# Optimization experiments

Measured on AMD Instinct MI355X. Metric: run time of the kernel, lower is better.

Reference implementation:

```python
import jax, jax.numpy as jnp
import numpy as np

B, C, NH = 2, 128, 4
H = W = D = 28
WS = 7
SHIFT = 3
N = WS * WS * WS            # 343 tokens per window
HD = C // NH                # 32
SCALE = HD ** -0.5
HIDDEN = int(C * 4.0)
EPS = 1e-5


def _rel_pos_index():
    coords = np.stack(np.meshgrid(np.arange(WS), np.arange(WS), np.arange(WS), indexing='ij'))
    cf = coords.reshape(3, -1)                      # (3, N)
    rel = cf[:, :, None] - cf[:, None, :]           # (3, N, N)
    rel = rel.transpose(1, 2, 0) + (WS - 1)         # (N, N, 3), shifted to >=0
    idx = rel[..., 0] * (2 * WS - 1) ** 2 + rel[..., 1] * (2 * WS - 1) + rel[..., 2]
    return jnp.asarray(idx, dtype=jnp.int32)        # (N, N)


def setup_inputs() -> dict:
    key = jax.random.key(0)
    ks = jax.random.split(key, 16)
    s = 0.02
    return {
        'x': jax.random.normal(ks[0], (B, H * W * D, C), jnp.float32),
        'norm1_w': jnp.ones((C,), jnp.float32),
        'norm1_b': jnp.zeros((C,), jnp.float32),
        'qkv_w': jax.random.normal(ks[1], (3 * C, C), jnp.float32) * s,
        'qkv_b': jnp.zeros((3 * C,), jnp.float32),
        'rpb_table': jax.random.normal(ks[2], ((2 * WS - 1) ** 3, NH), jnp.float32) * s,
        'proj_w': jax.random.normal(ks[3], (C, C), jnp.float32) * s,
        'proj_b': jnp.zeros((C,), jnp.float32),
        'norm2_w': jnp.ones((C,), jnp.float32),
        'norm2_b': jnp.zeros((C,), jnp.float32),
        'mlp_w1': jax.random.normal(ks[4], (HIDDEN, C), jnp.float32) * s,
        'mlp_b1': jnp.zeros((HIDDEN,), jnp.float32),
        'mlp_w2': jax.random.normal(ks[5], (C, HIDDEN), jnp.float32) * s,
        'mlp_b2': jnp.zeros((C,), jnp.float32),
        'rel_idx': _rel_pos_index(),
    }


def _layernorm(x, w, b):
    mu = jnp.mean(x, axis=-1, keepdims=True)
    var = jnp.mean(jnp.square(x - mu), axis=-1, keepdims=True)
    return (x - mu) * jax.lax.rsqrt(var + EPS) * w + b


def _window_partition(x):
    # (B,H,W,D,C) -> (B*nW, N, C)
    x = x.reshape(B, H // WS, WS, W // WS, WS, D // WS, WS, C)
    x = x.transpose(0, 1, 3, 5, 2, 4, 6, 7)
    return x.reshape(-1, N, C)


def _window_reverse(wins):
    # (B*nW, N, C) -> (B,H,W,D,C)
    x = wins.reshape(B, H // WS, W // WS, D // WS, WS, WS, WS, C)
    x = x.transpose(0, 1, 4, 2, 5, 3, 6, 7)
    return x.reshape(B, H, W, D, C)


def _window_attention(xw, qkv_w, qkv_b, rpb_table, rel_idx, proj_w, proj_b):
    Bw = xw.shape[0]
    qkv = xw @ qkv_w.T + qkv_b                       # (Bw, N, 3C)
    qkv = qkv.reshape(Bw, N, 3, NH, HD).transpose(2, 0, 3, 1, 4)
    q, k, v = qkv[0], qkv[1], qkv[2]                 # each (Bw, NH, N, HD)
    attn = jnp.einsum('bhnd,bhmd->bhnm', q * SCALE, k)
    bias = rpb_table[rel_idx.reshape(-1)].reshape(N, N, NH).transpose(2, 0, 1)
    attn = jax.nn.softmax(attn + bias[None], axis=-1)
    out = jnp.einsum('bhnm,bhmd->bhnd', attn, v)     # (Bw, NH, N, HD)
    out = out.transpose(0, 2, 1, 3).reshape(Bw, N, C)
    return out @ proj_w.T + proj_b


def reference(x, norm1_w, norm1_b, qkv_w, qkv_b, rpb_table, proj_w, proj_b,
              norm2_w, norm2_b, mlp_w1, mlp_b1, mlp_w2, mlp_b2, rel_idx):
    shortcut = x
    h = _layernorm(x, norm1_w, norm1_b).reshape(B, H, W, D, C)
    if SHIFT > 0:
        h = jnp.roll(h, shift=(-SHIFT, -SHIFT, -SHIFT), axis=(1, 2, 3))
    wins = _window_partition(h)
    wins = _window_attention(wins, qkv_w, qkv_b, rpb_table, rel_idx, proj_w, proj_b)
    h = _window_reverse(wins)
    if SHIFT > 0:
        h = jnp.roll(h, shift=(SHIFT, SHIFT, SHIFT), axis=(1, 2, 3))
    x = shortcut + h.reshape(B, H * W * D, C)
    m = _layernorm(x, norm2_w, norm2_b)
    m = jax.nn.gelu(m @ mlp_w1.T + mlp_b1, approximate=False) @ mlp_w2.T + mlp_b2
    return x + m
```

## Files before the change

kernel.cpp:

```cpp
#include <hip/hip_runtime.h>

typedef __bf16 bfv8 __attribute__((ext_vector_type(8)));
typedef float f32x4 __attribute__((ext_vector_type(4)));
#define MFMA16(a,b,c) __builtin_amdgcn_mfma_f32_16x16x32_bf16(a,b,c,0,0,0)

constexpr int C      = 128;
constexpr int HD     = 32;
constexpr int NTOK   = 343;
constexpr int ROWS   = 43904;
constexpr int HIDDEN = 512;
constexpr float SCALE = 0.17677669529663687f;
constexpr float EPS   = 1e-5f;
constexpr int NT = 22;

static __device__ __forceinline__ float b2f(ushort u) {
  union { unsigned int i; float f; } x; x.i = ((unsigned int)u) << 16; return x.f;
}
static __device__ __forceinline__ ushort f2b(float f) {
  union { float f; unsigned int i; } x; x.f = f;
  unsigned int r = x.i + 0x7fffu + ((x.i >> 16) & 1u);
  return (ushort)(r >> 16);
}

static __device__ __forceinline__ int perm_row(int row) {
  int win = row / NTOK, tok = row - win * NTOK;
  int bb = win >> 6, wi = win & 63;
  int a  = wi >> 4, w2 = (wi >> 2) & 3, c2 = wi & 3;
  int t1 = tok / 49, rem = tok - t1 * 49;
  int t2 = rem / 7,  t3 = rem - t2 * 7;
  int gh = a * 7 + t1 + 3;  if (gh >= 28) gh -= 28;
  int gw = w2 * 7 + t2 + 3; if (gw >= 28) gw -= 28;
  int gd = c2 * 7 + t3 + 3; if (gd >= 28) gd -= 28;
  return bb * 21952 + gh * 784 + gw * 28 + gd;
}

__global__ __launch_bounds__(256) void cvt_kernel(const float* __restrict__ s0,
                                                  const float* __restrict__ s1,
                                                  const float* __restrict__ s2,
                                                  const float* __restrict__ s3,
                                                  ushort* __restrict__ d0,
                                                  ushort* __restrict__ d1,
                                                  ushort* __restrict__ d2,
                                                  ushort* __restrict__ d3) {
  int t = blockIdx.x * 256 + threadIdx.x;
  if (t < 49152)       d0[t]          = f2b(s0[t]);
  else if (t < 65536)  d1[t - 49152]  = f2b(s1[t - 49152]);
  else if (t < 131072) d2[t - 65536]  = f2b(s2[t - 65536]);
  else                 d3[t - 131072] = f2b(s3[t - 131072]);
}

__global__ __launch_bounds__(256) void bias_kernel(const int* __restrict__ rel,
                                                   const float* __restrict__ tab,
                                                   float4* __restrict__ biasr) {
  int t = blockIdx.x * 256 + threadIdx.x;
  if (t >= 4 * NT * NT * 64) return;
  int lane = t & 63;
  int nt   = (t >> 6) % NT;
  int mt   = ((t >> 6) / NT) % NT;
  int head = t / (64 * NT * NT);
  int k  = nt * 16 + (lane & 15);
  int qb = mt * 16 + (lane >> 4) * 4;
  float vv[4];
  #pragma unroll
  for (int r = 0; r < 4; ++r) {
    int q = qb + r;
    if (q < NTOK && k < NTOK) {
      int idx = rel[q * NTOK + k];
      vv[r] = tab[idx * 4 + head];
    } else {
      vv[r] = -3e38f;
    }
  }
  biasr[t] = make_float4(vv[0], vv[1], vv[2], vv[3]);
}

template<bool PERM>
__global__ __launch_bounds__(256) void ln_kernel(const float* __restrict__ in,
                                                 const float* __restrict__ w,
                                                 const float* __restrict__ b,
                                                 ushort* __restrict__ out) {
  int wid = threadIdx.x >> 6, lane = threadIdx.x & 63;
  int row = blockIdx.x * 4 + wid;
  int src = PERM ? perm_row(row) : row;
  float2 v = *reinterpret_cast<const float2*>(in + (size_t)src * C + lane * 2);
  float s = v.x + v.y, q = v.x * v.x + v.y * v.y;
  #pragma unroll
  for (int off = 32; off; off >>= 1) { s += __shfl_xor(s, off); q += __shfl_xor(q, off); }
  float mu = s * (1.0f / 128.0f);
  float var = q * (1.0f / 128.0f) - mu * mu;
  float rs = rsqrtf(var + EPS);
  int c = lane * 2;
  ushort2 ov;
  ov.x = f2b((v.x - mu) * rs * w[c]     + b[c]);
  ov.y = f2b((v.y - mu) * rs * w[c + 1] + b[c + 1]);
  *reinterpret_cast<ushort2*>(out + (size_t)row * C + c) = ov;
}

template<int KTOT, int EPI>
__global__ __launch_bounds__(256) void gemm_kernel(const ushort* __restrict__ A,
                                                   const ushort* __restrict__ W,
                                                   const float* __restrict__ bias,
                                                   const float* __restrict__ X,
                                                   ushort* __restrict__ O0,
                                                   ushort* __restrict__ O1,
                                                   ushort* __restrict__ O2,
                                                   float* __restrict__ OF) {
  __shared__ ushort Al[128][136];
  __shared__ ushort Bl[128][136];
  const int m0 = blockIdx.x * 128, n0 = blockIdx.y * 128;
  const int tid = threadIdx.x, lane = tid & 63, wid = tid >> 6;
  const int wr = wid >> 1, wc = wid & 1;
  const int lr = lane & 15, kb0 = (lane >> 4) * 8;
  const int sr = tid >> 4, sc = (tid & 15) * 8;
  f32x4 acc[4][4] = {};
  for (int kc = 0; kc < KTOT; kc += 128) {
    #pragma unroll
    for (int p = 0; p < 8; ++p) {
      int row = p * 16 + sr;
      *reinterpret_cast<int4*>(&Al[row][sc]) =
          *reinterpret_cast<const int4*>(&A[(size_t)(m0 + row) * KTOT + kc + sc]);
      *reinterpret_cast<int4*>(&Bl[row][sc]) =
          *reinterpret_cast<const int4*>(&W[(size_t)(n0 + row) * KTOT + kc + sc]);
    }
    __syncthreads();
    #pragma unroll
    for (int kk = 0; kk < 4; ++kk) {
      int kb = kk * 32 + kb0;
      bfv8 a[4], b[4];
      #pragma unroll
      for (int m = 0; m < 4; ++m) a[m] = *reinterpret_cast<const bfv8*>(&Al[wr * 64 + m * 16 + lr][kb]);
      #pragma unroll
      for (int n = 0; n < 4; ++n) b[n] = *reinterpret_cast<const bfv8*>(&Bl[wc * 64 + n * 16 + lr][kb]);
      #pragma unroll
      for (int m = 0; m < 4; ++m)
        #pragma unroll
        for (int n = 0; n < 4; ++n)
          acc[m][n] = MFMA16(a[m], b[n], acc[m][n]);
    }
    __syncthreads();
  }
  #pragma unroll
  for (int m = 0; m < 4; ++m)
    #pragma unroll
    for (int n = 0; n < 4; ++n)
      #pragma unroll
      for (int r = 0; r < 4; ++r) {
        int gm = m0 + wr * 64 + m * 16 + (lane >> 4) * 4 + r;
        int gn = n0 + wc * 64 + n * 16 + (lane & 15);
        float v = acc[m][n][r] + bias[gn];
        if (EPI == 0) {
          int which = gn >> 7, head = (gn >> 5) & 3, d = gn & 31;
          if (which == 0) v *= SCALE;
          int win = gm / NTOK, tok = gm - win * NTOK;
          ushort* dst = (which == 0) ? O0 : (which == 1) ? O1 : O2;
          dst[((win * 4 + head) * NTOK + tok) * HD + d] = f2b(v);
        } else if (EPI == 1) {
          int orig = perm_row(gm);
          OF[(size_t)orig * C + gn] = v + X[(size_t)orig * C + gn];
        } else if (EPI == 2) {
          float g = 0.5f * v * (1.0f + erff(v * 0.70710678118654752f));
          O0[(size_t)gm * HIDDEN + gn] = f2b(g);
        } else {
          OF[(size_t)gm * C + gn] = v + X[(size_t)gm * C + gn];
        }
      }
}

__global__ __launch_bounds__(512) void attn_kernel(const ushort* __restrict__ Q,
                                                   const ushort* __restrict__ K,
                                                   const ushort* __restrict__ V,
                                                   const f32x4* __restrict__ biasr,
                                                   ushort* __restrict__ out) {
  __shared__ ushort vt[32][360];
  __shared__ ushort pl[8][16][204];
  const int wh = blockIdx.x;
  const int win = wh >> 2, head = wh & 3;
  const int tid = threadIdx.x, lane = tid & 63, wave = tid >> 6;
  if (tid < 352) {
    int t = tid;
    if (t < NTOK) {
      ushort tmp[32];
      const ushort* vr = V + ((size_t)wh * NTOK + t) * HD;
      *reinterpret_cast<int4*>(&tmp[0])  = *reinterpret_cast<const int4*>(vr);
      *reinterpret_cast<int4*>(&tmp[8])  = *reinterpret_cast<const int4*>(vr + 8);
      *reinterpret_cast<int4*>(&tmp[16]) = *reinterpret_cast<const int4*>(vr + 16);
      *reinterpret_cast<int4*>(&tmp[24]) = *reinterpret_cast<const int4*>(vr + 24);
      #pragma unroll
      for (int d = 0; d < 32; ++d) vt[d][t] = tmp[d];
    } else {
      #pragma unroll
      for (int d = 0; d < 32; ++d) vt[d][t] = 0;
    }
  }
  __syncthreads();
  const int lr = lane & 15, kb0 = (lane >> 4) * 8;
  const int key = lane & 15, qr4 = (lane >> 4) * 4;
  for (int mt = wave; mt < NT; mt += 8) {
    int qrow = mt * 16 + lr; if (qrow > 342) qrow = 342;
    bfv8 aq = *reinterpret_cast<const bfv8*>(Q + ((size_t)wh * NTOK + qrow) * HD + kb0);
    const f32x4* bR = biasr + ((size_t)(head * NT + mt) * NT) * 64 + lane;
    float sm[4] = {0.f, 0.f, 0.f, 0.f};
    f32x4 o0 = {}, o1 = {};
    #pragma unroll
    for (int nt = 0; nt < 12; ++nt) {
      int krow = nt * 16 + lr;
      bfv8 bk = *reinterpret_cast<const bfv8*>(K + ((size_t)wh * NTOK + krow) * HD + kb0);
      f32x4 s = MFMA16(aq, bk, bR[nt * 64]);
      int kcol = nt * 16 + key;
      #pragma unroll
      for (int r = 0; r < 4; ++r) {
        float p = __expf(s[r]);
        sm[r] += p;
        pl[wave][qr4 + r][kcol] = f2b(p);
      }
    }
    #pragma unroll
    for (int kt = 0; kt < 6; ++kt) {
      bfv8 bp  = *reinterpret_cast<const bfv8*>(&pl[wave][lr][kt * 32 + kb0]);
      bfv8 av0 = *reinterpret_cast<const bfv8*>(&vt[lr][kt * 32 + kb0]);
      bfv8 av1 = *reinterpret_cast<const bfv8*>(&vt[16 + lr][kt * 32 + kb0]);
      o0 = MFMA16(av0, bp, o0);
      o1 = MFMA16(av1, bp, o1);
    }
    #pragma unroll
    for (int nt = 12; nt < NT; ++nt) {
      int krow = nt * 16 + lr; if (krow > 342) krow = 342;
      bfv8 bk = *reinterpret_cast<const bfv8*>(K + ((size_t)wh * NTOK + krow) * HD + kb0);
      f32x4 s = MFMA16(aq, bk, bR[nt * 64]);
      int kcol = (nt - 12) * 16 + key;
      #pragma unroll
      for (int r = 0; r < 4; ++r) {
        float p = __expf(s[r]);
        sm[r] += p;
        pl[wave][qr4 + r][kcol] = f2b(p);
      }
    }
    #pragma unroll
    for (int kt = 0; kt < 5; ++kt) {
      bfv8 bp  = *reinterpret_cast<const bfv8*>(&pl[wave][lr][kt * 32 + kb0]);
      bfv8 av0 = *reinterpret_cast<const bfv8*>(&vt[lr][192 + kt * 32 + kb0]);
      bfv8 av1 = *reinterpret_cast<const bfv8*>(&vt[16 + lr][192 + kt * 32 + kb0]);
      o0 = MFMA16(av0, bp, o0);
      o1 = MFMA16(av1, bp, o1);
    }
    #pragma unroll
    for (int r = 0; r < 4; ++r) {
      #pragma unroll
      for (int off = 1; off < 16; off <<= 1) sm[r] += __shfl_xor(sm[r], off);
    }
    float inv[4];
    #pragma unroll
    for (int r = 0; r < 4; ++r) inv[r] = 1.0f / sm[r];
    int qcol = lane & 15;
    int srcl = (qcol >> 2) << 4;
    float i0 = __shfl(inv[0], srcl), i1 = __shfl(inv[1], srcl);
    float i2 = __shfl(inv[2], srcl), i3 = __shfl(inv[3], srcl);
    float invq = (qcol & 2) ? ((qcol & 1) ? i3 : i2) : ((qcol & 1) ? i1 : i0);
    int q = mt * 16 + qcol;
    if (q < NTOK) {
      int dbase = qr4;
      ushort4 r0, r1;
      r0.x = f2b(o0[0] * invq); r0.y = f2b(o0[1] * invq);
      r0.z = f2b(o0[2] * invq); r0.w = f2b(o0[3] * invq);
      r1.x = f2b(o1[0] * invq); r1.y = f2b(o1[1] * invq);
      r1.z = f2b(o1[2] * invq); r1.w = f2b(o1[3] * invq);
      ushort* ob = out + (size_t)(win * NTOK + q) * C + head * HD;
      *reinterpret_cast<ushort4*>(ob + dbase)      = r0;
      *reinterpret_cast<ushort4*>(ob + 16 + dbase) = r1;
    }
  }
}

extern "C" void kernel_launch(void* const* d_in, const int* in_sizes, int n_in,
                              void* d_out, int out_size, void* d_ws, size_t ws_size,
                              hipStream_t stream) {
  const float* x     = (const float*)d_in[0];
  const float* n1w   = (const float*)d_in[1];
  const float* n1b   = (const float*)d_in[2];
  const float* qkvw  = (const float*)d_in[3];
  const float* qkvb  = (const float*)d_in[4];
  const float* rpb   = (const float*)d_in[5];
  const float* projw = (const float*)d_in[6];
  const float* projb = (const float*)d_in[7];
  const float* n2w   = (const float*)d_in[8];
  const float* n2b   = (const float*)d_in[9];
  const float* w1    = (const float*)d_in[10];
  const float* b1    = (const float*)d_in[11];
  const float* w2    = (const float*)d_in[12];
  const float* b2    = (const float*)d_in[13];
  const int*   rel   = (const int*)d_in[14];

  char* ws = (char*)d_ws;
  constexpr size_t SZ_ACT  = (size_t)ROWS * C * 2;
  constexpr size_t SZ_BIAS = (size_t)4 * NT * NT * 64 * 16;

  ushort* lnbuf  = (ushort*)(ws);
  ushort* Qb     = (ushort*)(ws + SZ_ACT);
  ushort* Kb     = (ushort*)(ws + 2 * SZ_ACT);
  ushort* Vb     = (ushort*)(ws + 3 * SZ_ACT);
  f32x4*  biasr  = (f32x4*)(ws + 4 * SZ_ACT);
  size_t off_att = (4 * SZ_ACT + SZ_BIAS + 255) & ~(size_t)255;
  ushort* attout = (ushort*)(ws + off_att);
  ushort* h1     = Qb;
  size_t off_y   = off_att + SZ_ACT;
  float*  y      = (float*)(ws + off_y);
  size_t off_w   = off_y + (size_t)ROWS * C * 4;
  ushort* wqkv   = (ushort*)(ws + off_w);
  ushort* wproj  = (ushort*)(ws + off_w + 98304);
  ushort* wm1    = (ushort*)(ws + off_w + 131072);
  ushort* wm2    = (ushort*)(ws + off_w + 262144);
  float*  outp   = (float*)d_out;

  cvt_kernel<<<768, 256, 0, stream>>>(qkvw, projw, w1, w2, wqkv, wproj, wm1, wm2);
  bias_kernel<<<(4 * NT * NT * 64 + 255) / 256, 256, 0, stream>>>(rel, rpb, (float4*)biasr);
  ln_kernel<true><<<ROWS / 4, 256, 0, stream>>>(x, n1w, n1b, lnbuf);
  gemm_kernel<128, 0><<<dim3(343, 3), 256, 0, stream>>>(lnbuf, wqkv, qkvb, nullptr, Qb, Kb, Vb, nullptr);
  attn_kernel<<<512, 512, 0, stream>>>(Qb, Kb, Vb, biasr, attout);
  gemm_kernel<128, 1><<<dim3(343, 1), 256, 0, stream>>>(attout, wproj, projb, x, nullptr, nullptr, nullptr, y);
  ln_kernel<false><<<ROWS / 4, 256, 0, stream>>>(y, n2w, n2b, lnbuf);
  gemm_kernel<128, 2><<<dim3(343, 4), 256, 0, stream>>>(lnbuf, wm1, b1, nullptr, h1, nullptr, nullptr, nullptr);
  gemm_kernel<512, 3><<<dim3(343, 1), 256, 0, stream>>>(h1, wm2, b2, y, nullptr, nullptr, nullptr, outp);
}
```

Baseline: 140.4 us.

## Fuse LayerNorm2, MLP fc1+GELU and fc2 with residual into one kernel

Replaces the second LayerNorm kernel and the two MLP GEMM launches with a single kernel. Each block normalizes 64 rows into LDS, then walks the hidden dimension in 128-wide chunks: it computes that fc1 chunk with GELU, keeps the result in LDS, and immediately accumulates it into the fc2 output. This removes the HBM round trips of the normalized activations and the 512-wide hidden tensor, plus two launches. In exchange it uses small 64-row tiles with one wave per 16 rows, reloads weights from global memory per block, and synchronizes often, which may lower MFMA utilization compared with the earlier 128-row GEMM tiles.

```diff
diff --git a/kernel.cpp b/kernel.cpp
--- a/kernel.cpp
+++ b/kernel.cpp
@@ -154,16 +154,127 @@
           int win = gm / NTOK, tok = gm - win * NTOK;
           ushort* dst = (which == 0) ? O0 : (which == 1) ? O1 : O2;
           dst[((win * 4 + head) * NTOK + tok) * HD + d] = f2b(v);
-        } else if (EPI == 1) {
+        } else {
           int orig = perm_row(gm);
           OF[(size_t)orig * C + gn] = v + X[(size_t)orig * C + gn];
-        } else if (EPI == 2) {
-          float g = 0.5f * v * (1.0f + erff(v * 0.70710678118654752f));
-          O0[(size_t)gm * HIDDEN + gn] = f2b(g);
-        } else {
-          OF[(size_t)gm * C + gn] = v + X[(size_t)gm * C + gn];
         }
       }
+}
+
+__global__ __launch_bounds__(256) void mlp_kernel(const float* __restrict__ y,
+                                                  const float* __restrict__ nw,
+                                                  const float* __restrict__ nb,
+                                                  const ushort* __restrict__ W1,
+                                                  const float* __restrict__ b1,
+                                                  const ushort* __restrict__ W2,
+                                                  const float* __restrict__ b2,
+                                                  float* __restrict__ outp) {
+  __shared__ ushort Al[64][136];
+  __shared__ ushort Hl[4][16][136];
+  __shared__ ushort Wl[128][136];
+  const int m0 = blockIdx.x * 64;
+  const int tid = threadIdx.x, lane = tid & 63, wave = tid >> 6;
+  {
+    int sub = tid & 7;
+    #pragma unroll
+    for (int p = 0; p < 2; ++p) {
+      int row = p * 32 + (tid >> 3);
+      const float* yr = y + (size_t)(m0 + row) * C + sub * 16;
+      float4 v0 = *reinterpret_cast<const float4*>(yr);
+      float4 v1 = *reinterpret_cast<const float4*>(yr + 4);
+      float4 v2 = *reinterpret_cast<const float4*>(yr + 8);
+      float4 v3 = *reinterpret_cast<const float4*>(yr + 12);
+      float s = v0.x + v0.y + v0.z + v0.w + v1.x + v1.y + v1.z + v1.w
+              + v2.x + v2.y + v2.z + v2.w + v3.x + v3.y + v3.z + v3.w;
+      float q = v0.x*v0.x + v0.y*v0.y + v0.z*v0.z + v0.w*v0.w
+              + v1.x*v1.x + v1.y*v1.y + v1.z*v1.z + v1.w*v1.w
+              + v2.x*v2.x + v2.y*v2.y + v2.z*v2.z + v2.w*v2.w
+              + v3.x*v3.x + v3.y*v3.y + v3.z*v3.z + v3.w*v3.w;
+      #pragma unroll
+      for (int off = 1; off < 8; off <<= 1) { s += __shfl_xor(s, off); q += __shfl_xor(q, off); }
+      float mu = s * (1.0f / 128.0f);
+      float var = q * (1.0f / 128.0f) - mu * mu;
+      float rs = rsqrtf(var + EPS);
+      int c0 = sub * 16;
+      float4 vv[4] = {v0, v1, v2, v3};
+      #pragma unroll
+      for (int j = 0; j < 4; ++j) {
+        int c = c0 + j * 4;
+        ushort4 o;
+        o.x = f2b((vv[j].x - mu) * rs * nw[c]     + nb[c]);
+        o.y = f2b((vv[j].y - mu) * rs * nw[c + 1] + nb[c + 1]);
+        o.z = f2b((vv[j].z - mu) * rs * nw[c + 2] + nb[c + 2]);
+        o.w = f2b((vv[j].w - mu) * rs * nw[c + 3] + nb[c + 3]);
+        *reinterpret_cast<ushort4*>(&Al[row][c]) = o;
+      }
+    }
+  }
+  __syncthreads();
+  const int lr = lane & 15, kb0 = (lane >> 4) * 8;
+  const int key = lane & 15, qr4 = (lane >> 4) * 4;
+  const int sr = tid >> 4, sc = (tid & 15) * 8;
+  bfv8 af[4];
+  #pragma unroll
+  for (int kk = 0; kk < 4; ++kk)
+    af[kk] = *reinterpret_cast<const bfv8*>(&Al[wave * 16 + lr][kk * 32 + kb0]);
+  f32x4 acc[8] = {};
+  for (int c = 0; c < 4; ++c) {
+    #pragma unroll
+    for (int p = 0; p < 8; ++p) {
+      int row = p * 16 + sr;
+      *reinterpret_cast<int4*>(&Wl[row][sc]) =
+          *reinterpret_cast<const int4*>(&W1[(size_t)(c * 128 + row) * 128 + sc]);
+    }
+    __syncthreads();
+    f32x4 hacc[8] = {};
+    #pragma unroll
+    for (int kk = 0; kk < 4; ++kk) {
+      bfv8 a = af[kk];
+      #pragma unroll
+      for (int n = 0; n < 8; ++n) {
+        bfv8 w = *reinterpret_cast<const bfv8*>(&Wl[n * 16 + lr][kk * 32 + kb0]);
+        hacc[n] = MFMA16(a, w, hacc[n]);
+      }
+    }
+    #pragma unroll
+    for (int n = 0; n < 8; ++n)
+      #pragma unroll
+      for (int r = 0; r < 4; ++r) {
+        float val = hacc[n][r] + b1[c * 128 + n * 16 + key];
+        float g = 0.5f * val * (1.0f + erff(val * 0.70710678118654752f));
+        Hl[wave][qr4 + r][n * 16 + key] = f2b(g);
+      }
+    bfv8 hf[4];
+    #pragma unroll
+    for (int kk = 0; kk < 4; ++kk)
+      hf[kk] = *reinterpret_cast<const bfv8*>(&Hl[wave][lr][kk * 32 + kb0]);
+    __syncthreads();
+    #pragma unroll
+    for (int p = 0; p < 8; ++p) {
+      int row = p * 16 + sr;
+      *reinterpret_cast<int4*>(&Wl[row][sc]) =
+          *reinterpret_cast<const int4*>(&W2[(size_t)row * HIDDEN + c * 128 + sc]);
+    }
+    __syncthreads();
+    #pragma unroll
+    for (int kk = 0; kk < 4; ++kk) {
+      bfv8 h = hf[kk];
+      #pragma unroll
+      for (int n = 0; n < 8; ++n) {
+        bfv8 w = *reinterpret_cast<const bfv8*>(&Wl[n * 16 + lr][kk * 32 + kb0]);
+        acc[n] = MFMA16(h, w, acc[n]);
+      }
+    }
+    __syncthreads();
+  }
+  #pragma unroll
+  for (int n = 0; n < 8; ++n)
+    #pragma unroll
+    for (int r = 0; r < 4; ++r) {
+      int gm = m0 + wave * 16 + qr4 + r;
+      int gn = n * 16 + key;
+      outp[(size_t)gm * C + gn] = acc[n][r] + b2[gn] + y[(size_t)gm * C + gn];
+    }
 }
 
 __global__ __launch_bounds__(512) void attn_kernel(const ushort* __restrict__ Q,
@@ -301,7 +412,6 @@
   f32x4*  biasr  = (f32x4*)(ws + 4 * SZ_ACT);
   size_t off_att = (4 * SZ_ACT + SZ_BIAS + 255) & ~(size_t)255;
   ushort* attout = (ushort*)(ws + off_att);
-  ushort* h1     = Qb;
   size_t off_y   = off_att + SZ_ACT;
   float*  y      = (float*)(ws + off_y);
   size_t off_w   = off_y + (size_t)ROWS * C * 4;
@@ -317,7 +427,5 @@
   gemm_kernel<128, 0><<<dim3(343, 3), 256, 0, stream>>>(lnbuf, wqkv, qkvb, nullptr, Qb, Kb, Vb, nullptr);
   attn_kernel<<<512, 512, 0, stream>>>(Qb, Kb, Vb, biasr, attout);
   gemm_kernel<128, 1><<<dim3(343, 1), 256, 0, stream>>>(attout, wproj, projb, x, nullptr, nullptr, nullptr, y);
-  ln_kernel<false><<<ROWS / 4, 256, 0, stream>>>(y, n2w, n2b, lnbuf);
-  gemm_kernel<128, 2><<<dim3(343, 4), 256, 0, stream>>>(lnbuf, wm1, b1, nullptr, h1, nullptr, nullptr, nullptr);
-  gemm_kernel<512, 3><<<dim3(343, 1), 256, 0, stream>>>(h1, wm2, b2, y, nullptr, nullptr, nullptr, outp);
-}
+  mlp_kernel<<<ROWS / 64, 256, 0, stream>>>(y, n2w, n2b, wm1, b1, wm2, b2, outp);
+}
```

Result: faster. 137.6 us (-2.0%).
